# Kernel tuning notes

Hardware: AMD Instinct MI355X
Metric: run time of the kernel (lower is better)

Reference implementation:

```python
import jax, jax.numpy as jnp
import numpy as np

B, L, C, H, V = 64, 512, 256, 4, 32000
D = C // H
DIL = (1, 2, 4)
WIN = 3
NC = (50, 20)
NEG = -1e9


def setup_inputs() -> dict:
    key = jax.random.key(0)
    ks = jax.random.split(key, 20)
    g = lambda i, shape: jax.random.normal(ks[i], shape, jnp.float32) * 0.05
    Lay = len(DIL)
    x = jax.random.randint(ks[0], (B, L), 0, V)
    emb = g(1, (V, C)).at[0].set(0.0)  # padding_idx=0 row is zero
    return dict(
        x=x, emb=emb, pos=g(2, (L, C)),
        gp_W=g(3, (Lay, C, C)), gp_as=g(4, (Lay, H, D)), gp_ad=g(5, (Lay, H, D)),
        gf_W=g(6, (Lay, C, C)), gf_as=g(7, (Lay, H, D)), gf_ad=g(8, (Lay, H, D)),
        msg_W=g(9, (Lay, C, 2 * C)), msg_b=jnp.zeros((Lay, C), jnp.float32),
        gru_Wih=g(10, (Lay, 3 * C, C)), gru_bih=jnp.zeros((Lay, 3 * C), jnp.float32),
        gru_Whh=g(11, (Lay, 3 * C, C)), gru_bhh=jnp.zeros((Lay, 3 * C), jnp.float32),
        ln_g=jnp.ones((Lay, C), jnp.float32), ln_b=jnp.zeros((Lay, C), jnp.float32),
        pool_w=g(12, (C,)), pool_b=jnp.zeros((), jnp.float32),
        h0_W=g(13, (NC[0], C)), h0_b=jnp.zeros((NC[0],), jnp.float32),
        h1_W=g(14, (NC[1], C)), h1_b=jnp.zeros((NC[1],), jnp.float32),
    )


def _dense_gat(x, W, a_src, a_dst, adj):
    # x: [B,L,C], W: [C_out,C_in], a_*: [H,D], adj: [B,L,L] bool
    b, l, _ = x.shape
    h = jnp.einsum('blc,oc->blo', x, W).reshape(b, l, H, D).transpose(0, 2, 1, 3)  # [B,H,L,D]
    s = jnp.einsum('bhld,hd->bhl', h, a_src)
    d = jnp.einsum('bhld,hd->bhl', h, a_dst)
    e = s[:, :, :, None] + d[:, :, None, :]            # [B,H,L,L]
    e = jnp.where(e > 0, e, 0.2 * e)                   # LeakyReLU(0.2)
    e = jnp.where(adj[:, None, :, :], e, NEG)
    alpha = jax.nn.softmax(e, axis=-1)                 # dropout is identity in eval
    out = jnp.einsum('bhij,bhjd->bhid', alpha, h)
    return out.transpose(0, 2, 1, 3).reshape(b, l, C)


def _forward(x, emb, pos, gp_W, gp_as, gp_ad, gf_W, gf_as, gf_ad,
             msg_W, msg_b, gru_Wih, gru_bih, gru_Whh, gru_bhh,
             ln_g, ln_b, pool_w, pool_b, h0_W, h0_b, h1_W, h1_b):
    mask = x != 0                                      # [B,L]
    mf = mask.astype(jnp.float32)[..., None]           # [B,L,1]
    h = (emb[x] + pos[None, :, :] * mf) * mf
    logical = jnp.clip(jnp.cumsum(mask.astype(jnp.int32), axis=1) - 1, 0)
    valid = mask[:, None, :] & mask[:, :, None]        # [B,L,L]
    eye = jnp.eye(L, dtype=bool)[None]
    for l in range(len(DIL)):
        dil = DIL[l]
        diff = logical[:, :, None] - logical[:, None, :]
        ad = jnp.abs(diff)
        in_win = (ad <= WIN * dil) & (ad % dil == 0)
        adj_p = (valid & in_win & (diff < 0)) | eye
        adj_f = (valid & in_win & (diff > 0)) | eye
        m_p = _dense_gat(h, gp_W[l], gp_as[l], gp_ad[l], adj_p)
        m_f = _dense_gat(h, gf_W[l], gf_as[l], gf_ad[l], adj_f)
        m = jnp.concatenate([m_p, m_f], axis=-1)
        m = jax.nn.relu(jnp.einsum('blk,ck->blc', m, msg_W[l]) + msg_b[l])
        # GRUCell(input=m, hidden=h), PyTorch gate order: r,z,n
        gi = jnp.einsum('blc,gc->blg', m, gru_Wih[l]) + gru_bih[l]
        gh = jnp.einsum('blc,gc->blg', h, gru_Whh[l]) + gru_bhh[l]
        ir, iz, inn = jnp.split(gi, 3, axis=-1)
        hr, hz, hn = jnp.split(gh, 3, axis=-1)
        r = jax.nn.sigmoid(ir + hr)
        z = jax.nn.sigmoid(iz + hz)
        n = jnp.tanh(inn + r * hn)
        h_new = (1.0 - z) * n + z * h
        mu = jnp.mean(h_new, axis=-1, keepdims=True)
        var = jnp.mean(jnp.square(h_new - mu), axis=-1, keepdims=True)
        h_new = (h_new - mu) * jax.lax.rsqrt(var + 1e-5) * ln_g[l] + ln_b[l]
        h = h_new * mf
    # attention pooling over sequence (masked softmax on linear scores)
    sc = jnp.einsum('blc,c->bl', h, pool_w) + pool_b
    sc = jnp.where(mask, sc, NEG)
    a = jax.nn.softmax(sc, axis=-1)
    pooled = jnp.einsum('bl,blc->bc', a, h)            # dropout identity in eval
    o0 = pooled @ h0_W.T + h0_b
    o1 = pooled @ h1_W.T + h1_b
    return jnp.concatenate([o0, o1], axis=-1)          # [B, 50+20]


def reference(x, emb, pos, gp_W, gp_as, gp_ad, gf_W, gf_as, gf_ad,
              msg_W, msg_b, gru_Wih, gru_bih, gru_Whh, gru_bhh,
              ln_g, ln_b, pool_w, pool_b, h0_W, h0_b, h1_W, h1_b):
    return _forward(x, emb, pos, gp_W, gp_as, gp_ad, gf_W, gf_as, gf_ad,
                    msg_W, msg_b, gru_Wih, gru_bih, gru_Whh, gru_bhh,
                    ln_g, ln_b, pool_w, pool_b, h0_W, h0_b, h1_W, h1_b)
```

## Files before the change

### kernel.cpp

```cpp
#include <hip/hip_runtime.h>
#include <math.h>

#define B_ 64
#define L_ 512
#define C_ 256
#define H_ 4
#define LAY 3
#define NEGV -1e9f

#define GF_BIAS  1
#define GF_RELU  2
#define GF_OBF16 4

typedef __attribute__((ext_vector_type(8))) short short8;
typedef __attribute__((ext_vector_type(4))) short short4v;
typedef __attribute__((ext_vector_type(4))) float floatx4;

static __device__ __forceinline__ float rcp_(float x) { return __builtin_amdgcn_rcpf(x); }
static __device__ __forceinline__ float sig_(float x) { return rcp_(1.f + __expf(-x)); }
static __device__ __forceinline__ float tanh_(float x) {
    float e = __expf(2.f * x);
    return 1.f - 2.f * rcp_(e + 1.f);
}

static __device__ __forceinline__ short f2bf(float f) {
    unsigned x = __float_as_uint(f);
    x += 0x7fffu + ((x >> 16) & 1u);
    return (short)(x >> 16);
}
static __device__ __forceinline__ float bf2f(short s) {
    return __uint_as_float(((unsigned)(unsigned short)s) << 16);
}

static __device__ __forceinline__ int tok_swizzle(int blk) {
    int c8 = blk & 7, i = blk >> 3;
    return (c8 + 8 * (i >> 5)) * 128 + (i & 31) * 4;
}

static __device__ __forceinline__ void gl_lds16(const short* g, short* l) {
    __builtin_amdgcn_global_load_lds(
        (const __attribute__((address_space(1))) unsigned int*)g,
        (__attribute__((address_space(3))) unsigned int*)l, 16, 0, 0);
}

#define CF() asm volatile("" ::: "memory")

__global__ void scan_kernel(const int* __restrict__ x, int* __restrict__ mask,
                            int* __restrict__ logical, int* __restrict__ pol,
                            int* __restrict__ nvalid) {
    int b = blockIdx.x, t = threadIdx.x;
    __shared__ int s[L_];
    int m = (x[b * L_ + t] != 0) ? 1 : 0;
    s[t] = m;
    __syncthreads();
    for (int off = 1; off < L_; off <<= 1) {
        int v = (t >= off) ? s[t - off] : 0;
        __syncthreads();
        s[t] += v;
        __syncthreads();
    }
    int cum = s[t];
    int lg = cum - 1; if (lg < 0) lg = 0;
    mask[b * L_ + t] = m;
    logical[b * L_ + t] = lg;
    if (m) pol[b * L_ + lg] = t;
    if (t == L_ - 1) nvalid[b] = cum;
}

__global__ void embed_kernel(const int* __restrict__ x, const float* __restrict__ emb,
                             const float* __restrict__ pos, short* __restrict__ hb) {
    int t = threadIdx.x;
    int bl = tok_swizzle(blockIdx.x) + (t >> 6);
    int lane = t & 63;
    int xv = x[bl];
    float mf = (xv != 0) ? 1.f : 0.f;
    int l = bl & (L_ - 1);
    float4 e = *(const float4*)&emb[(size_t)xv * C_ + lane * 4];
    float4 p = *(const float4*)&pos[(size_t)l * C_ + lane * 4];
    short4v hv4;
    hv4.x = f2bf((e.x + p.x * mf) * mf);
    hv4.y = f2bf((e.y + p.y * mf) * mf);
    hv4.z = f2bf((e.z + p.z * mf) * mf);
    hv4.w = f2bf((e.w + p.w * mf) * mf);
    *(short4v*)&hb[(size_t)bl * C_ + lane * 4] = hv4;
}

__global__ void f2bf_kernel(const float* __restrict__ s, short* __restrict__ d, int n) {
    int i = blockIdx.x * 256 + threadIdx.x;
    if (i < n) d[i] = f2bf(s[i]);
}

__global__ void prep_wcomb(const float* __restrict__ gpW, const float* __restrict__ gfW,
                           const float* __restrict__ gpas, const float* __restrict__ gpad,
                           const float* __restrict__ gfas, const float* __restrict__ gfad,
                           short* __restrict__ Wc) {
    int i = blockIdx.x * 256 + threadIdx.x;
    if (i >= 3 * 640 * 256) return;
    int k = i & 255;
    int r = (i >> 8) % 640;
    int l = i / (640 * 256);
    float v = 0.f;
    if (r < 256) {
        v = gpW[((size_t)l * 256 + r) * 256 + k];
    } else if (r < 512) {
        v = gfW[((size_t)l * 256 + (r - 256)) * 256 + k];
    } else {
        int n = r - 512;
        if (n < 16) {
            int type = n >> 3, dir = (n >> 2) & 1, hh = n & 3;
            const float* a = type ? (dir ? gfad : gpad) : (dir ? gfas : gpas);
            const float* W = dir ? gfW : gpW;
            for (int j = 0; j < 64; j++) {
                float av = a[l * 256 + hh * 64 + j];
                float wv = W[((size_t)l * 256 + hh * 64 + j) * 256 + k];
                v = fmaf(av, wv, v);
            }
        }
    }
    Wc[i] = f2bf(v);
}

__global__ void prep_gru_i(const float* __restrict__ Wih, const float* __restrict__ Whh,
                           short* __restrict__ Bc) {
    int i = blockIdx.x * 256 + threadIdx.x;
    if (i >= 3 * 1024 * 512) return;
    int k = i & 511, np = (i >> 9) & 1023, l = i >> 19;
    int ch = np >> 2, g = np & 3;
    float v = 0.f;
    if (g < 2) {
        v = (k < 256) ? Wih[((size_t)l * 768 + g * 256 + ch) * 256 + k]
                      : Whh[((size_t)l * 768 + g * 256 + ch) * 256 + (k - 256)];
    } else if (g == 2) {
        if (k < 256) v = Wih[((size_t)l * 768 + 512 + ch) * 256 + k];
    } else {
        if (k >= 256) v = Whh[((size_t)l * 768 + 512 + ch) * 256 + (k - 256)];
    }
    Bc[i] = f2bf(v);
}

__global__ void prep_bias4(const float* __restrict__ bih, const float* __restrict__ bhh,
                           float* __restrict__ bc) {
    int i = blockIdx.x * 256 + threadIdx.x;
    if (i >= 3 * 1024) return;
    int np = i & 1023, l = i >> 10;
    int ch = np >> 2, g = np & 3;
    float v;
    if (g < 2)       v = bih[l * 768 + g * 256 + ch] + bhh[l * 768 + g * 256 + ch];
    else if (g == 2) v = bih[l * 768 + 512 + ch];
    else             v = bhh[l * 768 + 512 + ch];
    bc[i] = v;
}

__global__ __launch_bounds__(256) void bgemm(const short* __restrict__ A0,
                                             const short* __restrict__ Bw,
                                             void* __restrict__ Cout,
                                             const float* __restrict__ bias,
                                             int K, int lda, int ldc, int nstore,
                                             int cbBits, int flags) {
    __shared__ short As[128 * 32];
    __shared__ short Bs[128 * 32];
    const int id = blockIdx.x;
    const int cb = (id >> 3) & ((1 << cbBits) - 1);
    const int rb = (id & 7) + ((id >> (3 + cbBits)) << 3);
    const int tid = threadIdx.x;
    const int wave = tid >> 6, lane = tid & 63;
    const int wm = wave >> 1, wn = wave & 1;
    const size_t arow0 = (size_t)rb * 128;
    const short* Bb = Bw + (size_t)cb * 128 * K;
    floatx4 acc[4][4];
#pragma unroll
    for (int i = 0; i < 4; i++)
#pragma unroll
        for (int j = 0; j < 4; j++) acc[i][j] = (floatx4)0.f;

    const int srow = lane >> 2;
    const int sq = (lane & 3) * 8;
    const int q = lane >> 4, t16 = lane & 15;

    for (int k0 = 0; k0 < K; k0 += 32) {
        const short* Abase = A0 + arow0 * (size_t)lda + k0;
#pragma unroll
        for (int t = 0; t < 2; ++t) {
            int r = (wave * 2 + t) * 16 + srow;
            gl_lds16(Abase + (size_t)r * lda + sq, &As[r * 32 + sq]);
            gl_lds16(Bb + (size_t)r * K + k0 + sq, &Bs[r * 32 + sq]);
        }
        __syncthreads();
        short8 af[4], bfr[4];
#pragma unroll
        for (int mf = 0; mf < 4; mf++)
            af[mf] = *(const short8*)&As[(wm * 64 + mf * 16 + t16) * 32 + q * 8];
#pragma unroll
        for (int nf = 0; nf < 4; nf++)
            bfr[nf] = *(const short8*)&Bs[(wn * 64 + nf * 16 + t16) * 32 + q * 8];
#pragma unroll
        for (int mf = 0; mf < 4; mf++)
#pragma unroll
            for (int nf = 0; nf < 4; nf++)
                acc[nf][mf] = __builtin_amdgcn_mfma_f32_16x16x32_bf16(
                    bfr[nf], af[mf], acc[nf][mf], 0, 0, 0);
        __syncthreads();
    }

    const int rowbase = rb * 128 + wm * 64;
    const int colbase = cb * 128 + wn * 64;
#pragma unroll
    for (int nf = 0; nf < 4; nf++) {
        int col0 = colbase + nf * 16 + q * 4;
        if (col0 >= nstore) continue;
        float4 bv4 = make_float4(0.f, 0.f, 0.f, 0.f);
        if (flags & GF_BIAS) bv4 = *(const float4*)&bias[col0];
#pragma unroll
        for (int mf = 0; mf < 4; mf++) {
            int row = rowbase + mf * 16 + t16;
            float v0 = acc[nf][mf][0] + bv4.x;
            float v1 = acc[nf][mf][1] + bv4.y;
            float v2 = acc[nf][mf][2] + bv4.z;
            float v3 = acc[nf][mf][3] + bv4.w;
            if (flags & GF_RELU) {
                v0 = fmaxf(v0, 0.f); v1 = fmaxf(v1, 0.f);
                v2 = fmaxf(v2, 0.f); v3 = fmaxf(v3, 0.f);
            }
            size_t base = (size_t)row * ldc + col0;
            if (flags & GF_OBF16) {
                short4v pk;
                pk.x = f2bf(v0); pk.y = f2bf(v1); pk.z = f2bf(v2); pk.w = f2bf(v3);
                *(short4v*)&((short*)Cout)[base] = pk;
            } else {
                float4 pk = make_float4(v0, v1, v2, v3);
                *(float4*)&((float*)Cout)[base] = pk;
            }
        }
    }
}

__global__ __launch_bounds__(256) void projssd_bgemm(const short* __restrict__ A0,
                                                     const short* __restrict__ Bw,
                                                     short* __restrict__ hpb2,
                                                     float* __restrict__ Ssd) {
    __shared__ short As[128 * 32];
    __shared__ short Bs[128 * 32];
    const int id = blockIdx.x;
    const int grp = id >> 3;
    const int cb = grp % 5;
    const int rb = (id & 7) + (grp / 5) * 8;
    const int tid = threadIdx.x;
    const int wave = tid >> 6, lane = tid & 63;
    const int wm = wave >> 1, wn = wave & 1;
    const size_t arow0 = (size_t)rb * 128;
    const short* Bb = Bw + (size_t)cb * 128 * 256;
    floatx4 acc[4][4];
#pragma unroll
    for (int i = 0; i < 4; i++)
#pragma unroll
        for (int j = 0; j < 4; j++) acc[i][j] = (floatx4)0.f;

    const int srow = lane >> 2;
    const int sq = (lane & 3) * 8;
    const int q = lane >> 4, t16 = lane & 15;

    for (int k0 = 0; k0 < 256; k0 += 32) {
        const short* Abase = A0 + arow0 * 256 + k0;
#pragma unroll
        for (int t = 0; t < 2; ++t) {
            int r = (wave * 2 + t) * 16 + srow;
            gl_lds16(Abase + (size_t)r * 256 + sq, &As[r * 32 + sq]);
            gl_lds16(Bb + (size_t)r * 256 + k0 + sq, &Bs[r * 32 + sq]);
        }
        __syncthreads();
        short8 af[4], bfr[4];
#pragma unroll
        for (int mf = 0; mf < 4; mf++)
            af[mf] = *(const short8*)&As[(wm * 64 + mf * 16 + t16) * 32 + q * 8];
#pragma unroll
        for (int nf = 0; nf < 4; nf++)
            bfr[nf] = *(const short8*)&Bs[(wn * 64 + nf * 16 + t16) * 32 + q * 8];
#pragma unroll
        for (int mf = 0; mf < 4; mf++)
#pragma unroll
            for (int nf = 0; nf < 4; nf++)
                acc[nf][mf] = __builtin_amdgcn_mfma_f32_16x16x32_bf16(
                    bfr[nf], af[mf], acc[nf][mf], 0, 0, 0);
        __syncthreads();
    }

    const int rowbase = rb * 128 + wm * 64;
    if (cb < 4) {
        const int colbase = cb * 128 + wn * 64;
#pragma unroll
        for (int nf = 0; nf < 4; nf++) {
            int col0 = colbase + nf * 16 + q * 4;
#pragma unroll
            for (int mf = 0; mf < 4; mf++) {
                int row = rowbase + mf * 16 + t16;
                short4v pk;
                pk.x = f2bf(acc[nf][mf][0]);
                pk.y = f2bf(acc[nf][mf][1]);
                pk.z = f2bf(acc[nf][mf][2]);
                pk.w = f2bf(acc[nf][mf][3]);
                *(short4v*)&hpb2[(size_t)row * 512 + col0] = pk;
            }
        }
    } else {
        if (wn == 0) {
            int col0 = q * 4;
            if (col0 < 16) {
#pragma unroll
                for (int mf = 0; mf < 4; mf++) {
                    int row = rowbase + mf * 16 + t16;
                    float4 pk = make_float4(acc[0][mf][0], acc[0][mf][1],
                                            acc[0][mf][2], acc[0][mf][3]);
                    *(float4*)&Ssd[(size_t)row * 16 + col0] = pk;
                }
            }
        }
    }
}

static __device__ __forceinline__ short8 lds_rd8(const short* p) {
    return *(const short8*)p;
}

template <int MH>
static __device__ __forceinline__ void ld_af(const short* bufA, int wm, int q, int t16,
                                             short8 af[4][2]) {
#pragma unroll
    for (int mfl = 0; mfl < 4; ++mfl) {
        int row = wm * 128 + (MH * 4 + mfl) * 16 + t16;
#pragma unroll
        for (int ks = 0; ks < 2; ++ks) {
            int cg = (ks * 4 + q) ^ (row & 7);
            af[mfl][ks] = lds_rd8(&bufA[row * 64 + cg * 8]);
        }
    }
}

template <int NH>
static __device__ __forceinline__ void ld_bf(const short* bufB, int wn, int q, int t16,
                                             short8 bf[2][2]) {
#pragma unroll
    for (int nfl = 0; nfl < 2; ++nfl) {
        int row = wn * 64 + (NH * 2 + nfl) * 16 + t16;
#pragma unroll
        for (int ks = 0; ks < 2; ++ks) {
            int cg = (ks * 4 + q) ^ (row & 7);
            bf[nfl][ks] = lds_rd8(&bufB[row * 64 + cg * 8]);
        }
    }
}

template <int MH, int NH>
static __device__ __forceinline__ void mfma_q(const short8 af[4][2], const short8 bf[2][2],
                                              floatx4 acc[4][8]) {
    __builtin_amdgcn_s_setprio(1);
#pragma unroll
    for (int ks = 0; ks < 2; ++ks)
#pragma unroll
        for (int mfl = 0; mfl < 4; ++mfl)
#pragma unroll
            for (int nfl = 0; nfl < 2; ++nfl)
                acc[NH * 2 + nfl][MH * 4 + mfl] = __builtin_amdgcn_mfma_f32_16x16x32_bf16(
                    bf[nfl][ks], af[mfl][ks], acc[NH * 2 + nfl][MH * 4 + mfl], 0, 0, 0);
    __builtin_amdgcn_s_setprio(0);
}

__global__ __launch_bounds__(512, 2) void gru_bgemm(const short* __restrict__ mmb,
                                                    const short* __restrict__ hb_in,
                                                    const short* __restrict__ Bw,
                                                    short* __restrict__ hn2b,
                                                    const float* __restrict__ bias4) {
    __shared__ short lds[2][32768];
    const int id = blockIdx.x;
    const int rb = 16 * (id & 7) + (id >> 5);
    const int cb = (id >> 3) & 3;
    const int tid = threadIdx.x;
    const int wave = tid >> 6, lane = tid & 63;
    const int wm = wave >> 2, wn = wave & 3;
    const int q = lane >> 4, t16 = lane & 15;
    const size_t arow0 = (size_t)rb * 256;
    const short* Bb = Bw + (size_t)cb * 256 * 512;

    floatx4 acc[4][8];
#pragma unroll
    for (int i = 0; i < 4; i++)
#pragma unroll
        for (int j = 0; j < 8; j++) acc[i][j] = (floatx4)0.f;

    auto stageA = [&](int tt, int Hh) {
        const short* Asrc = (tt < 4) ? (mmb + tt * 64) : (hb_in + (tt - 4) * 64);
        short* bufA = lds[tt & 1];
#pragma unroll
        for (int i = 0; i < 2; ++i) {
            int unit = i * 512 + tid;
            int row = Hh * 128 + (unit >> 3);
            int cs = (unit & 7) ^ (row & 7);
            gl_lds16(Asrc + (arow0 + (size_t)row) * 256 + cs * 8,
                     bufA + Hh * 8192 + unit * 8);
        }
    };
    auto stageB = [&](int tt, int Hh) {
        short* bufB = lds[tt & 1] + 16384;
#pragma unroll
        for (int i = 0; i < 2; ++i) {
            int unit = i * 512 + tid;
            int row = Hh * 128 + (unit >> 3);
            int cs = (unit & 7) ^ (row & 7);
            gl_lds16(Bb + (size_t)row * 512 + tt * 64 + cs * 8,
                     bufB + Hh * 8192 + unit * 8);
        }
    };

    stageA(0, 0); stageB(0, 0); stageA(0, 1); stageB(0, 1);
    stageA(1, 0); stageB(1, 0); stageA(1, 1); stageB(1, 1);
    asm volatile("s_waitcnt vmcnt(8)" ::: "memory");
    CF(); __builtin_amdgcn_s_barrier(); CF();

    short8 af[4][2], b0[2][2], b1[2][2];

#pragma unroll
    for (int t = 0; t < 8; ++t) {
        const short* bufA = lds[t & 1];
        const short* bufB = lds[t & 1] + 16384;

        ld_af<0>(bufA, wm, q, t16, af);
        ld_bf<0>(bufB, wn, q, t16, b0);
        if (t > 0 && t < 7) stageB(t + 1, 0);
        CF(); __builtin_amdgcn_s_barrier();
        asm volatile("s_waitcnt lgkmcnt(0)" ::: "memory");
        mfma_q<0, 0>(af, b0, acc);
        CF(); __builtin_amdgcn_s_barrier(); CF();

        ld_bf<1>(bufB, wn, q, t16, b1);
        if (t > 0 && t < 7) stageA(t + 1, 1);
        CF(); __builtin_amdgcn_s_barrier();
        asm volatile("s_waitcnt lgkmcnt(0)" ::: "memory");
        mfma_q<0, 1>(af, b1, acc);
        CF(); __builtin_amdgcn_s_barrier(); CF();

        ld_af<1>(bufA, wm, q, t16, af);
        if (t > 0 && t < 7) stageB(t + 1, 1);
        CF(); __builtin_amdgcn_s_barrier();
        asm volatile("s_waitcnt lgkmcnt(0)" ::: "memory");
        mfma_q<1, 1>(af, b1, acc);
        CF(); __builtin_amdgcn_s_barrier(); CF();

        if (t < 6) stageA(t + 2, 0);
        CF(); __builtin_amdgcn_s_barrier();
        mfma_q<1, 0>(af, b0, acc);
        if (t < 6)       asm volatile("s_waitcnt vmcnt(2)" ::: "memory");
        else if (t == 6) asm volatile("s_waitcnt vmcnt(0)" ::: "memory");
        CF(); __builtin_amdgcn_s_barrier(); CF();
    }

    short* sO = (short*)lds;
#pragma unroll
    for (int nf = 0; nf < 4; nf++) {
        int chl = wn * 16 + nf * 4 + q;
        int col0 = cb * 256 + wn * 64 + nf * 16 + q * 4;
        float4 bv4 = *(const float4*)&bias4[col0];
#pragma unroll
        for (int mf = 0; mf < 8; mf++) {
            int rowl = wm * 128 + mf * 16 + t16;
            size_t grow = arow0 + rowl;
            float r = sig_(acc[nf][mf][0] + bv4.x);
            float z = sig_(acc[nf][mf][1] + bv4.y);
            float nv = tanh_((acc[nf][mf][2] + bv4.z) + r * (acc[nf][mf][3] + bv4.w));
            float hp = bf2f(hb_in[grow * 256 + cb * 64 + chl]);
            sO[rowl * 72 + chl] = f2bf((1.f - z) * nv + z * hp);
        }
    }
    __syncthreads();
#pragma unroll
    for (int it = 0; it < 4; ++it) {
        int unit = it * 512 + tid;
        int rowl = unit >> 3, ck = unit & 7;
        *(short8*)&hn2b[(arow0 + rowl) * 256 + cb * 64 + ck * 8] =
            *(const short8*)&sO[rowl * 72 + ck * 8];
    }
}

__global__ __launch_bounds__(256) void ln_kernel(
    const short* __restrict__ hn2b, short* __restrict__ hb,
    const int* __restrict__ mask,
    const float* __restrict__ lng, const float* __restrict__ lnb) {
    int t = threadIdx.x;
    int bl = tok_swizzle(blockIdx.x) + (t >> 6);
    int lane = t & 63;
    short4v v4 = *(const short4v*)&hn2b[(size_t)bl * C_ + lane * 4];
    float v[4] = {bf2f(v4.x), bf2f(v4.y), bf2f(v4.z), bf2f(v4.w)};
    float s = (v[0] + v[1]) + (v[2] + v[3]);
    float ss = (v[0] * v[0] + v[1] * v[1]) + (v[2] * v[2] + v[3] * v[3]);
#pragma unroll
    for (int off = 32; off; off >>= 1) {
        s += __shfl_xor(s, off);
        ss += __shfl_xor(ss, off);
    }
    float mu = s * (1.f / 256.f);
    float var = ss * (1.f / 256.f) - mu * mu;
    float rstd = rsqrtf(fmaxf(var, 0.f) + 1e-5f);
    float4 lg = *(const float4*)&lng[lane * 4];
    float4 lb = *(const float4*)&lnb[lane * 4];
    float mfv = mask[bl] ? 1.f : 0.f;
    short4v yb;
    yb.x = f2bf(((v[0] - mu) * rstd * lg.x + lb.x) * mfv);
    yb.y = f2bf(((v[1] - mu) * rstd * lg.y + lb.y) * mfv);
    yb.z = f2bf(((v[2] - mu) * rstd * lg.z + lb.z) * mfv);
    yb.w = f2bf(((v[3] - mu) * rstd * lg.w + lb.w) * mfv);
    *(short4v*)&hb[(size_t)bl * C_ + lane * 4] = yb;
}

__global__ __launch_bounds__(256) void agg_fused(
    const short* __restrict__ hpb2, const float* __restrict__ S,
    const int* __restrict__ mask, const int* __restrict__ logical,
    const int* __restrict__ pol, const int* __restrict__ nvalid,
    short* __restrict__ m, int dil) {
    int t = threadIdx.x;
    int bl = tok_swizzle(blockIdx.x) + (t >> 6);
    int sub = t & 63;
    int dir = sub >> 5;
    int slot = sub & 31;
    int cb = slot * 8;
    int head = slot >> 3;
    int b = bl >> 9;

    int mi = mask[bl];
    int li = logical[bl];
    int nv = nvalid[b];
    int js[3]; int nn = 0;
    if (mi) {
#pragma unroll
        for (int k = 1; k <= 3; k++) {
            int lj = dir ? (li - k * dil) : (li + k * dil);
            if (lj >= 0 && lj < nv) js[nn++] = pol[b * L_ + lj];
        }
    }
    int sn = dir * 4 + head, dn = 8 + sn;
    float si = S[(size_t)bl * 16 + sn];
    float di = S[(size_t)bl * 16 + dn];
    float e0 = si + di; e0 = e0 > 0.f ? e0 : 0.2f * e0;
    float emax = e0, ev[3];
    for (int k = 0; k < nn; k++) {
        float djv = S[((size_t)(b * L_ + js[k])) * 16 + dn];
        float e = si + djv; e = e > 0.f ? e : 0.2f * e;
        ev[k] = e; emax = fmaxf(emax, e);
    }
    float w0 = __expf(e0 - emax), den = w0;
    float wv[3];
    for (int k = 0; k < nn; k++) { wv[k] = __expf(ev[k] - emax); den += wv[k]; }
    float rden = rcp_(den);

    size_t base = (size_t)bl * 512 + dir * 256 + cb;
    short8 vself = *(const short8*)&hpb2[base];
    float o[8];
#pragma unroll
    for (int j = 0; j < 8; j++) o[j] = w0 * bf2f(vself[j]);
    for (int k = 0; k < nn; k++) {
        short8 vn = *(const short8*)&hpb2[((size_t)(b * L_ + js[k])) * 512 + dir * 256 + cb];
#pragma unroll
        for (int j = 0; j < 8; j++) o[j] = fmaf(wv[k], bf2f(vn[j]), o[j]);
    }
    short8 ov;
#pragma unroll
    for (int j = 0; j < 8; j++) ov[j] = f2bf(o[j] * rden);
    *(short8*)&m[base] = ov;
}

__global__ __launch_bounds__(1024) void pool_head_kernel(
    const short* __restrict__ hb, const int* __restrict__ mask,
    const float* __restrict__ pw, const float* __restrict__ pb,
    const float* __restrict__ h0W, const float* __restrict__ h0b,
    const float* __restrict__ h1W, const float* __restrict__ h1b,
    float* __restrict__ out) {
    int b = blockIdx.x;
    int t = threadIdx.x;
    int lane = t & 63, wave = t >> 6;
    __shared__ float sc[L_];
    __shared__ float red[20];
    __shared__ float part[4][C_];
    __shared__ float pooled[C_];

    float4 wv = *(const float4*)&pw[lane * 4];
    for (int l = wave; l < L_; l += 16) {
        short4v hv = *(const short4v*)&hb[((size_t)b * L_ + l) * C_ + lane * 4];
        float p = bf2f(hv.x) * wv.x + bf2f(hv.y) * wv.y
                + bf2f(hv.z) * wv.z + bf2f(hv.w) * wv.w;
#pragma unroll
        for (int off = 32; off; off >>= 1) p += __shfl_down(p, off);
        if (lane == 0) sc[l] = mask[b * L_ + l] ? (p + pb[0]) : NEGV;
    }
    __syncthreads();

    float v = (t < L_) ? sc[t] : NEGV;
    float mx = v;
#pragma unroll
    for (int off = 32; off; off >>= 1) mx = fmaxf(mx, __shfl_down(mx, off));
    if (lane == 0) red[wave] = mx;
    __syncthreads();
    if (t == 0) {
        float g = red[0];
        for (int i = 1; i < 16; i++) g = fmaxf(g, red[i]);
        red[16] = g;
    }
    __syncthreads();
    float gmax = red[16];
    float e = (t < L_) ? __expf(v - gmax) : 0.f;
    float ssum = e;
#pragma unroll
    for (int off = 32; off; off >>= 1) ssum += __shfl_down(ssum, off);
    if (lane == 0) red[wave] = ssum;
    __syncthreads();
    if (t == 0) {
        float g = 0.f;
        for (int i = 0; i < 16; i++) g += red[i];
        red[17] = 1.f / g;
    }
    __syncthreads();
    if (t < L_) sc[t] = e * red[17];
    __syncthreads();

    int g = t >> 8, c = t & 255;
    const short* hrow = &hb[((size_t)b * L_ + g * 128) * C_ + c];
    const float* scg = &sc[g * 128];
    float a0 = 0.f, a1 = 0.f, a2 = 0.f, a3 = 0.f;
    for (int l = 0; l < 128; l += 4) {
        a0 = fmaf(scg[l + 0], bf2f(hrow[(size_t)(l + 0) * C_]), a0);
        a1 = fmaf(scg[l + 1], bf2f(hrow[(size_t)(l + 1) * C_]), a1);
        a2 = fmaf(scg[l + 2], bf2f(hrow[(size_t)(l + 2) * C_]), a2);
        a3 = fmaf(scg[l + 3], bf2f(hrow[(size_t)(l + 3) * C_]), a3);
    }
    part[g][c] = (a0 + a1) + (a2 + a3);
    __syncthreads();
    if (t < C_) pooled[t] = (part[0][t] + part[1][t]) + (part[2][t] + part[3][t]);
    __syncthreads();

    for (int o = wave; o < 70; o += 16) {
        const float* W = (o < 50) ? (h0W + (size_t)o * C_) : (h1W + (size_t)(o - 50) * C_);
        float bb = (o < 50) ? h0b[o] : h1b[o - 50];
        float4 w4 = *(const float4*)&W[lane * 4];
        float4 p4 = *(const float4*)&pooled[lane * 4];
        float s = p4.x * w4.x + p4.y * w4.y + p4.z * w4.z + p4.w * w4.w;
#pragma unroll
        for (int off = 32; off; off >>= 1) s += __shfl_down(s, off);
        if (lane == 0) out[b * 70 + o] = s + bb;
    }
}

extern "C" void kernel_launch(void* const* d_in, const int* in_sizes, int n_in,
                              void* d_out, int out_size, void* d_ws, size_t ws_size,
                              hipStream_t stream) {
    const int*   x    = (const int*)d_in[0];
    const float* emb  = (const float*)d_in[1];
    const float* pos  = (const float*)d_in[2];
    const float* gpW  = (const float*)d_in[3];
    const float* gpas = (const float*)d_in[4];
    const float* gpad = (const float*)d_in[5];
    const float* gfW  = (const float*)d_in[6];
    const float* gfas = (const float*)d_in[7];
    const float* gfad = (const float*)d_in[8];
    const float* msgW = (const float*)d_in[9];
    const float* msgb = (const float*)d_in[10];
    const float* Wih  = (const float*)d_in[11];
    const float* bih  = (const float*)d_in[12];
    const float* Whh  = (const float*)d_in[13];
    const float* bhh  = (const float*)d_in[14];
    const float* lng  = (const float*)d_in[15];
    const float* lnb  = (const float*)d_in[16];
    const float* pw   = (const float*)d_in[17];
    const float* pb   = (const float*)d_in[18];
    const float* h0W  = (const float*)d_in[19];
    const float* h0b  = (const float*)d_in[20];
    const float* h1W  = (const float*)d_in[21];
    const float* h1b  = (const float*)d_in[22];
    float* out = (float*)d_out;

    const size_t MW = 1024 * 1024;
    float* ws = (float*)d_ws;
    short* hn2b = (short*)ws;
    short* hb   = (short*)(ws + 8 * MW);
    short* mmb  = (short*)(ws + 12 * MW);
    float* Ssd  = ws + 12 * MW;
    short* hpb2 = (short*)(ws + 16 * MW);
    short* mb   = (short*)(ws + 24 * MW);
    short* Wcomb = (short*)(ws + 32 * MW);
    short* msgWb = Wcomb + 3 * 640 * 256;
    short* Bcat  = msgWb + 3 * 256 * 512;
    float* bias4 = (float*)(Bcat + 3 * 1024 * 512);
    int* mask    = (int*)(bias4 + 3 * 1024);
    int* logical = mask + B_ * L_;
    int* pol     = logical + B_ * L_;
    int* nvalid  = pol + B_ * L_;

    prep_wcomb<<<(3 * 640 * 256 + 255) / 256, 256, 0, stream>>>(gpW, gfW, gpas, gpad,
                                                                gfas, gfad, Wcomb);
    f2bf_kernel<<<(3 * 256 * 512 + 255) / 256, 256, 0, stream>>>(msgW, msgWb, 3 * 256 * 512);
    prep_gru_i<<<(3 * 1024 * 512 + 255) / 256, 256, 0, stream>>>(Wih, Whh, Bcat);
    prep_bias4<<<12, 256, 0, stream>>>(bih, bhh, bias4);

    scan_kernel<<<B_, L_, 0, stream>>>(x, mask, logical, pol, nvalid);
    embed_kernel<<<B_ * L_ / 4, 256, 0, stream>>>(x, emb, pos, hb);

    const int DILS[LAY] = {1, 2, 4};

    for (int l = 0; l < LAY; l++) {
        int dil = DILS[l];
        projssd_bgemm<<<256 * 5, 256, 0, stream>>>(hb, Wcomb + (size_t)l * 640 * 256,
                                                   hpb2, Ssd);
        agg_fused<<<8192, 256, 0, stream>>>(hpb2, Ssd, mask, logical, pol, nvalid, mb, dil);
        bgemm<<<256 * 2, 256, 0, stream>>>(mb, msgWb + (size_t)l * 256 * 512,
                                           mmb, msgb + l * C_, 512, 512, 256, 256, 1,
                                           GF_BIAS | GF_RELU | GF_OBF16);
        gru_bgemm<<<512, 512, 0, stream>>>(mmb, hb, Bcat + (size_t)l * 1024 * 512,
                                           hn2b, bias4 + l * 1024);
        ln_kernel<<<8192, 256, 0, stream>>>(hn2b, hb, mask, lng + l * C_, lnb + l * C_);
    }

    pool_head_kernel<<<B_, 1024, 0, stream>>>(hb, mask, pw, pb, h0W, h0b, h1W, h1b, out);
}
```

Baseline: 539.6 us.

## Remap GEMM block order, stagger GRU k-tile order, reuse staged h from LDS

The bgemm and projssd kernels now map block ids column-block-major with row blocks spread across the low bits, which changes L2/MALL locality and how blocks are spread across XCDs. The GRU GEMM rotates its k-tile order per column block, so the final staged tile is this block's own slice of the previous hidden state. The epilogue then reads h_prev from LDS instead of global memory. Prefetch is restructured to issue whole A/B tiles two steps ahead with a deeper vmcnt wait, and sched_barriers are added. This may shift load timing and register pressure.

```diff
diff --git a/kernel.cpp b/kernel.cpp
--- a/kernel.cpp
+++ b/kernel.cpp
@@ -160,8 +160,10 @@
     __shared__ short As[128 * 32];
     __shared__ short Bs[128 * 32];
     const int id = blockIdx.x;
-    const int cb = (id >> 3) & ((1 << cbBits) - 1);
-    const int rb = (id & 7) + ((id >> (3 + cbBits)) << 3);
+    const int nrb8 = gridDim.x >> (3 + cbBits);
+    const int j = id >> 3;
+    const int cb = j / nrb8;
+    const int rb = (id & 7) * nrb8 + (j % nrb8);
     const int tid = threadIdx.x;
     const int wave = tid >> 6, lane = tid & 63;
     const int wm = wave >> 1, wn = wave & 1;
@@ -171,7 +173,7 @@
 #pragma unroll
     for (int i = 0; i < 4; i++)
 #pragma unroll
-        for (int j = 0; j < 4; j++) acc[i][j] = (floatx4)0.f;
+        for (int jj = 0; jj < 4; jj++) acc[i][jj] = (floatx4)0.f;
 
     const int srow = lane >> 2;
     const int sq = (lane & 3) * 8;
@@ -241,9 +243,9 @@
     __shared__ short As[128 * 32];
     __shared__ short Bs[128 * 32];
     const int id = blockIdx.x;
-    const int grp = id >> 3;
-    const int cb = grp % 5;
-    const int rb = (id & 7) + (grp / 5) * 8;
+    const int j = id >> 3;
+    const int cb = j >> 5;
+    const int rb = ((id & 7) << 5) + (j & 31);
     const int tid = threadIdx.x;
     const int wave = tid >> 6, lane = tid & 63;
     const int wm = wave >> 1, wn = wave & 1;
@@ -253,7 +255,7 @@
 #pragma unroll
     for (int i = 0; i < 4; i++)
 #pragma unroll
-        for (int j = 0; j < 4; j++) acc[i][j] = (floatx4)0.f;
+        for (int jj = 0; jj < 4; jj++) acc[i][jj] = (floatx4)0.f;
 
     const int srow = lane >> 2;
     const int sq = (lane & 3) * 8;
@@ -379,30 +381,33 @@
     const int q = lane >> 4, t16 = lane & 15;
     const size_t arow0 = (size_t)rb * 256;
     const short* Bb = Bw + (size_t)cb * 256 * 512;
+    const int ord0 = (5 + cb) & 7;
 
     floatx4 acc[4][8];
 #pragma unroll
     for (int i = 0; i < 4; i++)
 #pragma unroll
-        for (int j = 0; j < 8; j++) acc[i][j] = (floatx4)0.f;
-
-    auto stageA = [&](int tt, int Hh) {
+        for (int jj = 0; jj < 8; jj++) acc[i][jj] = (floatx4)0.f;
+
+    auto stageA = [&](int i, int Hh) {
+        int tt = (ord0 + i) & 7;
         const short* Asrc = (tt < 4) ? (mmb + tt * 64) : (hb_in + (tt - 4) * 64);
-        short* bufA = lds[tt & 1];
-#pragma unroll
-        for (int i = 0; i < 2; ++i) {
-            int unit = i * 512 + tid;
+        short* bufA = lds[i & 1];
+#pragma unroll
+        for (int u = 0; u < 2; ++u) {
+            int unit = u * 512 + tid;
             int row = Hh * 128 + (unit >> 3);
             int cs = (unit & 7) ^ (row & 7);
             gl_lds16(Asrc + (arow0 + (size_t)row) * 256 + cs * 8,
                      bufA + Hh * 8192 + unit * 8);
         }
     };
-    auto stageB = [&](int tt, int Hh) {
-        short* bufB = lds[tt & 1] + 16384;
-#pragma unroll
-        for (int i = 0; i < 2; ++i) {
-            int unit = i * 512 + tid;
+    auto stageB = [&](int i, int Hh) {
+        int tt = (ord0 + i) & 7;
+        short* bufB = lds[i & 1] + 16384;
+#pragma unroll
+        for (int u = 0; u < 2; ++u) {
+            int unit = u * 512 + tid;
             int row = Hh * 128 + (unit >> 3);
             int cs = (unit & 7) ^ (row & 7);
             gl_lds16(Bb + (size_t)row * 512 + tt * 64 + cs * 8,
@@ -410,8 +415,8 @@
         }
     };
 
-    stageA(0, 0); stageB(0, 0); stageA(0, 1); stageB(0, 1);
-    stageA(1, 0); stageB(1, 0); stageA(1, 1); stageB(1, 1);
+    stageA(0, 0); stageA(0, 1); stageB(0, 0); stageB(0, 1);
+    stageA(1, 0); stageA(1, 1); stageB(1, 0); stageB(1, 1);
     asm volatile("s_waitcnt vmcnt(8)" ::: "memory");
     CF(); __builtin_amdgcn_s_barrier(); CF();
 
@@ -424,34 +429,36 @@
 
         ld_af<0>(bufA, wm, q, t16, af);
         ld_bf<0>(bufB, wn, q, t16, b0);
-        if (t > 0 && t < 7) stageB(t + 1, 0);
         CF(); __builtin_amdgcn_s_barrier();
         asm volatile("s_waitcnt lgkmcnt(0)" ::: "memory");
+        __builtin_amdgcn_sched_barrier(0);
         mfma_q<0, 0>(af, b0, acc);
         CF(); __builtin_amdgcn_s_barrier(); CF();
 
         ld_bf<1>(bufB, wn, q, t16, b1);
-        if (t > 0 && t < 7) stageA(t + 1, 1);
         CF(); __builtin_amdgcn_s_barrier();
         asm volatile("s_waitcnt lgkmcnt(0)" ::: "memory");
+        __builtin_amdgcn_sched_barrier(0);
         mfma_q<0, 1>(af, b1, acc);
         CF(); __builtin_amdgcn_s_barrier(); CF();
 
         ld_af<1>(bufA, wm, q, t16, af);
-        if (t > 0 && t < 7) stageB(t + 1, 1);
+        if (t < 6) { stageB(t + 2, 0); stageB(t + 2, 1); }
         CF(); __builtin_amdgcn_s_barrier();
         asm volatile("s_waitcnt lgkmcnt(0)" ::: "memory");
+        __builtin_amdgcn_sched_barrier(0);
         mfma_q<1, 1>(af, b1, acc);
         CF(); __builtin_amdgcn_s_barrier(); CF();
 
-        if (t < 6) stageA(t + 2, 0);
+        if (t < 6) { stageA(t + 2, 0); stageA(t + 2, 1); }
         CF(); __builtin_amdgcn_s_barrier();
         mfma_q<1, 0>(af, b0, acc);
-        if (t < 6)       asm volatile("s_waitcnt vmcnt(2)" ::: "memory");
+        if (t < 6)       asm volatile("s_waitcnt vmcnt(8)" ::: "memory");
         else if (t == 6) asm volatile("s_waitcnt vmcnt(0)" ::: "memory");
         CF(); __builtin_amdgcn_s_barrier(); CF();
     }
 
+    const short* hpt = lds[1];
     short* sO = (short*)lds;
 #pragma unroll
     for (int nf = 0; nf < 4; nf++) {
@@ -461,11 +468,10 @@
 #pragma unroll
         for (int mf = 0; mf < 8; mf++) {
             int rowl = wm * 128 + mf * 16 + t16;
-            size_t grow = arow0 + rowl;
+            float hp = bf2f(hpt[rowl * 64 + (((chl >> 3) ^ (rowl & 7)) << 3) + (chl & 7)]);
             float r = sig_(acc[nf][mf][0] + bv4.x);
             float z = sig_(acc[nf][mf][1] + bv4.y);
             float nv = tanh_((acc[nf][mf][2] + bv4.z) + r * (acc[nf][mf][3] + bv4.w));
-            float hp = bf2f(hb_in[grow * 256 + cb * 64 + chl]);
             sO[rowl * 72 + chl] = f2bf((1.f - z) * nv + z * hp);
         }
     }
```

Result: faster. 513.4 us (-4.9%).
